# Optimization experiments

Measured on AMD Instinct MI355X. Metric: run time of the kernel, lower is better.

## Reference

```python
import jax, jax.numpy as jnp
import numpy as np

N_NODES = 50000
N_EDGES = 800000
C = 256
R = 4

def setup_inputs() -> dict:
    key = jax.random.key(0)
    ks = jax.random.split(key, 8)
    node_features = jax.random.normal(ks[0], (N_NODES, C), dtype=jnp.float32)
    edge_index = jax.random.randint(ks[1], (2, N_EDGES), 0, N_NODES, dtype=jnp.int64)
    edge_type = jax.random.randint(ks[2], (N_EDGES,), 0, R, dtype=jnp.int64)
    # RGCNConv params (glorot-ish scale)
    s = 1.0 / np.sqrt(C)
    rel_weight = jax.random.normal(ks[3], (R, C, C), dtype=jnp.float32) * s
    root_weight = jax.random.normal(ks[4], (C, C), dtype=jnp.float32) * s
    rgcn_bias = jax.random.normal(ks[5], (C,), dtype=jnp.float32) * 0.01
    att_weight = jax.random.normal(ks[6], (1, 2 * C), dtype=jnp.float32) * (1.0 / np.sqrt(2 * C))
    att_bias = jax.random.normal(ks[7], (1,), dtype=jnp.float32) * 0.01
    return {
        'node_features': node_features,
        'edge_index': edge_index,
        'edge_type': edge_type,
        'rel_weight': rel_weight,
        'root_weight': root_weight,
        'rgcn_bias': rgcn_bias,
        'att_weight': att_weight,
        'att_bias': att_bias,
    }


def _rgcn(node_features, edge_index, edge_type, rel_weight, root_weight, rgcn_bias):
    # PyG RGCNConv: per-relation mean aggregation of x_src @ W_r, plus root transform + bias.
    N = node_features.shape[0]
    src, dst = edge_index[0], edge_index[1]
    out = node_features @ root_weight + rgcn_bias  # [N, O]
    num_rel = rel_weight.shape[0]
    for r in range(num_rel):  # small fixed relation count
        trans = node_features @ rel_weight[r]          # [N, O] node-level transform
        mask = (edge_type == r)
        msg = jnp.where(mask[:, None], trans[src], 0.0)  # [E, O] masked gather
        ssum = jax.ops.segment_sum(msg, dst, num_segments=N)
        cnt = jax.ops.segment_sum(mask.astype(node_features.dtype), dst, num_segments=N)
        out = out + ssum / jnp.maximum(cnt, 1.0)[:, None]  # mean aggr; 0 where no edges
    return out


def reference(node_features, edge_index, edge_type, rel_weight, root_weight, rgcn_bias, att_weight, att_bias):
    u0 = _rgcn(node_features, edge_index, edge_type, rel_weight, root_weight, rgcn_bias)
    cat = jnp.concatenate([u0, node_features], axis=1)  # [N, 2O]
    a = jax.nn.sigmoid(cat @ att_weight.T + att_bias)   # [N, 1]
    h = jnp.tanh(u0) * a + node_features * (1.0 - a)
    return h
```

## Files before the change

kernel.cpp:

```cpp
#include <hip/hip_runtime.h>
#include <hip/hip_bf16.h>

#define C 256
#define NOUT 1280
#define BK 32

typedef __attribute__((ext_vector_type(8))) short bf16x8;
typedef __attribute__((ext_vector_type(4))) float f32x4;
typedef __attribute__((ext_vector_type(4))) unsigned short us4;

#define GLL16(g, l)                                                         \
  __builtin_amdgcn_global_load_lds(                                         \
      (const __attribute__((address_space(1))) void*)(g),                   \
      (__attribute__((address_space(3))) void*)(l), 16, 0, 0)

__device__ __forceinline__ float bf2f(unsigned short u) {
  return __uint_as_float(((unsigned int)u) << 16);
}
__device__ __forceinline__ unsigned short f2bf(float f) {
  unsigned int x = __float_as_uint(f);
  unsigned int lsb = (x >> 16) & 1u;
  x += 0x7fffu + lsb;
  return (unsigned short)(x >> 16);
}

__global__ void k_pre(const float* __restrict__ X, const float* __restrict__ rel,
                      const float* __restrict__ root, const float* __restrict__ attw,
                      unsigned short* __restrict__ Xbf, unsigned short* __restrict__ WT2,
                      float* __restrict__ ax2, int* __restrict__ cnt,
                      int N, int rowsPad) {
  __shared__ float tw[64][65];
  int b = blockIdx.x, t = threadIdx.x;
  if (b < 80) {
    int m = b >> 4, tile = b & 15;
    int ti = tile >> 2, tj = tile & 3;
    const float* W = (m == 0) ? root : (rel + (size_t)(m - 1) * C * C);
    int row = t >> 2, cj = (t & 3) * 16;
    const float* src = W + (size_t)(ti * 64 + row) * C + tj * 64 + cj;
#pragma unroll
    for (int j = 0; j < 4; ++j) {
      float4 v = reinterpret_cast<const float4*>(src)[j];
      tw[row][cj + j * 4 + 0] = v.x;
      tw[row][cj + j * 4 + 1] = v.y;
      tw[row][cj + j * 4 + 2] = v.z;
      tw[row][cj + j * 4 + 3] = v.w;
    }
    __syncthreads();
    int c = t >> 2, k0 = (t & 3) * 16;
    int n = m * 256 + tj * 64 + c;
    unsigned short o[16];
#pragma unroll
    for (int k = 0; k < 16; ++k) o[k] = f2bf(tw[k0 + k][c]);
#pragma unroll
    for (int j = 0; j < 4; ++j)
      *reinterpret_cast<us4*>(WT2 + (size_t)n * C + ti * 64 + k0 + j * 4) =
          *reinterpret_cast<us4*>(&o[j * 4]);
  } else if (b < 80 + (rowsPad >> 2)) {
    int row = (b - 80) * 4 + (t >> 6);
    int lane = t & 63;
    if (row < N) {
      float4 v = reinterpret_cast<const float4*>(X + (size_t)row * C)[lane];
      float4 w2 = reinterpret_cast<const float4*>(attw + C)[lane];
      us4 o;
      o.x = f2bf(v.x); o.y = f2bf(v.y); o.z = f2bf(v.z); o.w = f2bf(v.w);
      reinterpret_cast<us4*>(Xbf)[(size_t)row * 64 + lane] = o;
      float p = v.x * w2.x + v.y * w2.y + v.z * w2.z + v.w * w2.w;
#pragma unroll
      for (int m2 = 32; m2 >= 1; m2 >>= 1) p += __shfl_xor(p, m2);
      if (lane == 0) ax2[row] = p;
    } else if (row < rowsPad) {
      us4 z; z.x = 0; z.y = 0; z.z = 0; z.w = 0;
      reinterpret_cast<us4*>(Xbf)[(size_t)row * 64 + lane] = z;
      if (lane == 0) ax2[row] = 0.f;
    }
  } else {
    int i = (b - 80 - (rowsPad >> 2)) * 256 + t;
    if (i < N) cnt[i] = 0;
  }
}

__global__ void k_hist(const int* __restrict__ edst, int* __restrict__ cnt, int E) {
  int e = blockIdx.x * blockDim.x + threadIdx.x;
  if (e < E) atomicAdd(cnt + edst[e], 1);
}

__global__ void k_scan1(const int* __restrict__ cnt, int* __restrict__ rp,
                        int* __restrict__ bsum, int n) {
  __shared__ int s[512];
  int t = threadIdx.x;
  int i = blockIdx.x * 512 + t;
  int v = (i < n) ? cnt[i] : 0;
  s[t] = v;
  __syncthreads();
  for (int off = 1; off < 512; off <<= 1) {
    int add = (t >= off) ? s[t - off] : 0;
    __syncthreads();
    s[t] += add;
    __syncthreads();
  }
  if (i < n) rp[i] = s[t] - v;
  if (t == 511) bsum[blockIdx.x] = s[511];
}

__global__ void k_scan2(const int* __restrict__ bsum, int* __restrict__ boff,
                        int* __restrict__ rp, int nb, int n) {
  if (threadIdx.x == 0) {
    int run = 0;
    for (int b = 0; b < nb; ++b) { boff[b] = run; run += bsum[b]; }
    rp[n] = run;
  }
}

__global__ void k_scan3(int* __restrict__ rp, const int* __restrict__ boff,
                        int* __restrict__ cursor, int n) {
  int i = blockIdx.x * 512 + threadIdx.x;
  if (i < n) {
    int v = rp[i] + boff[blockIdx.x];
    rp[i] = v;
    cursor[i] = v;
  }
}

__global__ void k_fill(const int* __restrict__ esrc, const int* __restrict__ edst,
                       const int* __restrict__ etype, int* __restrict__ cursor,
                       unsigned int* __restrict__ sorted, int E) {
  int e = blockIdx.x * blockDim.x + threadIdx.x;
  if (e >= E) return;
  int d = edst[e];
  int pos = atomicAdd(cursor + d, 1);
  sorted[pos] = (unsigned int)esrc[e] | ((unsigned int)etype[e] << 28);
}

__global__ __launch_bounds__(256) void k_gemm(
    const unsigned short* __restrict__ Xbf, const unsigned short* __restrict__ WT2,
    unsigned short* __restrict__ Y, int rowsPad) {
  __shared__ unsigned short smem[16384];
  unsigned short* ldsA = smem;
  unsigned short* ldsB = smem + 8192;
  int tid = threadIdx.x;
  int wave = tid >> 6, lane = tid & 63;

  int nwg = gridDim.x, orig = blockIdx.x;
  int q = nwg >> 3, r = nwg & 7;
  int xcd = orig & 7, lin = orig >> 3;
  int wgid = (xcd < r ? xcd * (q + 1) : r * (q + 1) + (xcd - r) * q) + lin;
  int mblk = wgid / 10, nblk = wgid - mblk * 10;
  int row0 = mblk * 128, col0 = nblk * 128;
  int wr = wave >> 1, wc = wave & 1, lcol = lane & 15;

  const unsigned short* aSrc[2];
  const unsigned short* bSrc[2];
  int ldsOfs[2];
#pragma unroll
  for (int c2 = 0; c2 < 2; ++c2) {
    int off = (wave * 2 + c2) * 1024 + lane * 16;
    int rr = off >> 6;
    int lg8 = (((off >> 4) & 3) ^ ((rr >> 1) & 3)) * 8;
    aSrc[c2] = Xbf + (size_t)(row0 + rr) * C + lg8;
    bSrc[c2] = WT2 + (size_t)(col0 + rr) * C + lg8;
    ldsOfs[c2] = (wave * 2 + c2) * 1024;
  }

  int aoff[4], boff[4];
  int kb = (lane >> 4) * 16;
#pragma unroll
  for (int i = 0; i < 4; ++i) {
    int ar = wr * 64 + i * 16 + lcol;
    aoff[i] = ar * 64 + (kb ^ (((ar >> 1) & 3) << 4));
    int bc = wc * 64 + i * 16 + lcol;
    boff[i] = bc * 64 + (kb ^ (((bc >> 1) & 3) << 4));
  }

  f32x4 acc[4][4];
#pragma unroll
  for (int i = 0; i < 4; ++i)
#pragma unroll
    for (int j = 0; j < 4; ++j) {
      f32x4 z; z[0] = 0.f; z[1] = 0.f; z[2] = 0.f; z[3] = 0.f;
      acc[i][j] = z;
    }

  auto stage = [&](int buf, int ks) {
    int kofs = ks * BK;
#pragma unroll
    for (int c2 = 0; c2 < 2; ++c2) {
      GLL16(aSrc[c2] + kofs, (char*)(ldsA + buf * 4096) + ldsOfs[c2]);
      GLL16(bSrc[c2] + kofs, (char*)(ldsB + buf * 4096) + ldsOfs[c2]);
    }
  };

  stage(0, 0);
  __syncthreads();

#pragma unroll
  for (int ks = 0; ks < 8; ++ks) {
    int cur = ks & 1;
    if (ks + 1 < 8) stage(cur ^ 1, ks + 1);
    bf16x8 af[4], bfr[4];
#pragma unroll
    for (int i = 0; i < 4; ++i) {
      af[i]  = *reinterpret_cast<const bf16x8*>((const char*)(ldsA + cur * 4096) + aoff[i]);
      bfr[i] = *reinterpret_cast<const bf16x8*>((const char*)(ldsB + cur * 4096) + boff[i]);
    }
#pragma unroll
    for (int mr = 0; mr < 4; ++mr)
#pragma unroll
      for (int nc = 0; nc < 4; ++nc)
        acc[mr][nc] = __builtin_amdgcn_mfma_f32_16x16x32_bf16(af[mr], bfr[nc], acc[mr][nc], 0, 0, 0);
    __syncthreads();
  }

  int lrow4 = (lane >> 4) * 4;
#pragma unroll
  for (int mr = 0; mr < 4; ++mr)
#pragma unroll
    for (int nc = 0; nc < 4; ++nc)
#pragma unroll
      for (int reg = 0; reg < 4; ++reg) {
        int rr = wr * 64 + mr * 16 + lrow4 + reg;
        int cc = wc * 64 + nc * 16 + lcol;
        smem[rr * 128 + ((((cc >> 3) + rr) & 15) << 3) + (cc & 7)] =
            f2bf(acc[mr][nc][reg]);
      }
  __syncthreads();
#pragma unroll
  for (int rnd = 0; rnd < 8; ++rnd) {
    int rr = rnd * 16 + (tid >> 4);
    int g = tid & 15;
    int p = (g + rr) & 15;
    bf16x8 v = *reinterpret_cast<const bf16x8*>(smem + rr * 128 + p * 8);
    *reinterpret_cast<bf16x8*>(Y + (size_t)(row0 + rr) * NOUT + col0 + g * 8) = v;
  }
}

#define ACC(u, v)                                                            \
  do {                                                                       \
    float f0 = bf2f((v).x), f1 = bf2f((v).y), f2 = bf2f((v).z), f3 = bf2f((v).w); \
    switch ((u) >> 28) {                                                     \
      case 0: a0.x += f0; a0.y += f1; a0.z += f2; a0.w += f3; ++c0; break;   \
      case 1: a1.x += f0; a1.y += f1; a1.z += f2; a1.w += f3; ++c1; break;   \
      case 2: a2.x += f0; a2.y += f1; a2.z += f2; a2.w += f3; ++c2; break;   \
      default: a3.x += f0; a3.y += f1; a3.z += f2; a3.w += f3; ++c3; break;  \
    }                                                                        \
  } while (0)

__global__ void k_gg(const unsigned short* __restrict__ Y,
                     const unsigned int* __restrict__ sorted,
                     const int* __restrict__ rp, const float* __restrict__ X,
                     const float* __restrict__ bias, const float* __restrict__ attw,
                     const float* __restrict__ abp, const float* __restrict__ ax2,
                     float* __restrict__ out, int N) {
  int wave = threadIdx.x >> 6, lane = threadIdx.x & 63;
  int dst = blockIdx.x * 4 + wave;
  if (dst >= N) return;
  const us4* Yv = reinterpret_cast<const us4*>(Y);

  float4 a0 = make_float4(0, 0, 0, 0), a1 = a0, a2 = a0, a3 = a0;
  int c0 = 0, c1 = 0, c2 = 0, c3 = 0;
  int s = rp[dst], e2 = rp[dst + 1];

#define YIDX(u) ((size_t)((u) & 0x0FFFFFFFu) * 320 + (((u) >> 28) + 1) * 64 + lane)
  int e = s;
  for (; e + 8 <= e2; e += 8) {
    unsigned int u0 = sorted[e],     u1 = sorted[e + 1], u2 = sorted[e + 2], u3 = sorted[e + 3];
    unsigned int u4 = sorted[e + 4], u5 = sorted[e + 5], u6 = sorted[e + 6], u7 = sorted[e + 7];
    us4 v0 = Yv[YIDX(u0)], v1 = Yv[YIDX(u1)], v2 = Yv[YIDX(u2)], v3 = Yv[YIDX(u3)];
    us4 v4 = Yv[YIDX(u4)], v5 = Yv[YIDX(u5)], v6 = Yv[YIDX(u6)], v7 = Yv[YIDX(u7)];
    ACC(u0, v0); ACC(u1, v1); ACC(u2, v2); ACC(u3, v3);
    ACC(u4, v4); ACC(u5, v5); ACC(u6, v6); ACC(u7, v7);
  }
  for (; e + 4 <= e2; e += 4) {
    unsigned int u0 = sorted[e], u1 = sorted[e + 1], u2 = sorted[e + 2], u3 = sorted[e + 3];
    us4 v0 = Yv[YIDX(u0)], v1 = Yv[YIDX(u1)], v2 = Yv[YIDX(u2)], v3 = Yv[YIDX(u3)];
    ACC(u0, v0); ACC(u1, v1); ACC(u2, v2); ACC(u3, v3);
  }
  for (; e < e2; ++e) {
    unsigned int u = sorted[e];
    us4 v = Yv[YIDX(u)];
    ACC(u, v);
  }
#undef YIDX

  float s0 = 1.0f / (float)max(c0, 1);
  float s1 = 1.0f / (float)max(c1, 1);
  float s2 = 1.0f / (float)max(c2, 1);
  float s3 = 1.0f / (float)max(c3, 1);
  us4 rt = Yv[(size_t)dst * 320 + lane];
  float4 bi = reinterpret_cast<const float4*>(bias)[lane];
  float4 w1 = reinterpret_cast<const float4*>(attw)[lane];
  float4 u0;
  u0.x = a0.x * s0 + a1.x * s1 + a2.x * s2 + a3.x * s3 + bf2f(rt.x) + bi.x;
  u0.y = a0.y * s0 + a1.y * s1 + a2.y * s2 + a3.y * s3 + bf2f(rt.y) + bi.y;
  u0.z = a0.z * s0 + a1.z * s1 + a2.z * s2 + a3.z * s3 + bf2f(rt.z) + bi.z;
  u0.w = a0.w * s0 + a1.w * s1 + a2.w * s2 + a3.w * s3 + bf2f(rt.w) + bi.w;

  float p = u0.x * w1.x + u0.y * w1.y + u0.z * w1.z + u0.w * w1.w;
#pragma unroll
  for (int m2 = 32; m2 >= 1; m2 >>= 1) p += __shfl_xor(p, m2);
  float a = 1.0f / (1.0f + expf(-(p + ax2[dst] + abp[0])));
  float b = 1.0f - a;
  float4 x4 = reinterpret_cast<const float4*>(X + (size_t)dst * C)[lane];
  float4 h;
  h.x = tanhf(u0.x) * a + x4.x * b;
  h.y = tanhf(u0.y) * a + x4.y * b;
  h.z = tanhf(u0.z) * a + x4.z * b;
  h.w = tanhf(u0.w) * a + x4.w * b;
  reinterpret_cast<float4*>(out + (size_t)dst * C)[lane] = h;
}

extern "C" void kernel_launch(void* const* d_in, const int* in_sizes, int n_in,
                              void* d_out, int out_size, void* d_ws, size_t ws_size,
                              hipStream_t stream) {
  const float* X     = (const float*)d_in[0];
  const int*   eidx  = (const int*)d_in[1];
  const int*   etype = (const int*)d_in[2];
  const float* rel   = (const float*)d_in[3];
  const float* root  = (const float*)d_in[4];
  const float* bias  = (const float*)d_in[5];
  const float* attw  = (const float*)d_in[6];
  const float* ab    = (const float*)d_in[7];
  float* out = (float*)d_out;

  int N = in_sizes[0] / C;
  int E = in_sizes[2];
  int rowsPad = ((N + 127) / 128) * 128;
  const int* esrc = eidx;
  const int* edst = eidx + E;

  char* w = (char*)d_ws;
  size_t off = 0;
  auto alloc = [&](size_t bytes) -> void* {
    void* p = w + off;
    off += (bytes + 255) & ~(size_t)255;
    return p;
  };
  unsigned short* Y    = (unsigned short*)alloc((size_t)rowsPad * NOUT * 2);
  unsigned short* Xbf  = (unsigned short*)alloc((size_t)rowsPad * C * 2);
  unsigned short* WT2  = (unsigned short*)alloc((size_t)NOUT * C * 2);
  float* ax2  = (float*)alloc((size_t)rowsPad * 4);
  int* cnt    = (int*)alloc((size_t)N * 4);
  int* rp     = (int*)alloc((size_t)(N + 1) * 4);
  int* cursor = (int*)alloc((size_t)N * 4);
  int* bsum   = (int*)alloc(1024);
  int* boffb  = (int*)alloc(1024);
  unsigned int* sorted = (unsigned int*)alloc((size_t)E * 4);

  int preBlocks = 80 + (rowsPad >> 2) + (N + 255) / 256;
  k_pre<<<preBlocks, 256, 0, stream>>>(X, rel, root, attw, Xbf, WT2, ax2, cnt, N, rowsPad);
  k_hist<<<(E + 255) / 256, 256, 0, stream>>>(edst, cnt, E);
  int NB = (N + 511) / 512;
  k_scan1<<<NB, 512, 0, stream>>>(cnt, rp, bsum, N);
  k_scan2<<<1, 64, 0, stream>>>(bsum, boffb, rp, NB, N);
  k_scan3<<<NB, 512, 0, stream>>>(rp, boffb, cursor, N);
  k_fill<<<(E + 255) / 256, 256, 0, stream>>>(esrc, edst, etype, cursor, sorted, E);
  k_gemm<<<(rowsPad / 128) * 10, 256, 0, stream>>>(Xbf, WT2, Y, rowsPad);
  k_gg<<<(N + 3) / 4, 256, 0, stream>>>(Y, sorted, rp, X, bias, attw, ab, ax2, out, N);
}
```

Measured before the change: 254.8 us.

## Sort edges by (dst, relation) and precompute gather offsets to drop per-edge switch

The CSR is now bucketed by destination and relation (4N segments), so per-relation counts come from row pointers rather than per-edge counting. The gather kernel keeps one accumulator and applies a per-edge mean weight picked with compares, removing the four-way switch and the extra accumulator registers. The sorted array now stores a precomputed Y element offset instead of a packed src|type word. In exchange the histogram, scan and cursor arrays grow fourfold, and the scan must now cover 200k entries.

After: 251.8 us. About the same (-1.2%).

```diff
diff --git a/kernel.cpp b/kernel.cpp
--- a/kernel.cpp
+++ b/kernel.cpp
@@ -75,13 +75,14 @@
     }
   } else {
     int i = (b - 80 - (rowsPad >> 2)) * 256 + t;
-    if (i < N) cnt[i] = 0;
-  }
-}
-
-__global__ void k_hist(const int* __restrict__ edst, int* __restrict__ cnt, int E) {
+    if (i < 4 * N) cnt[i] = 0;
+  }
+}
+
+__global__ void k_hist(const int* __restrict__ edst, const int* __restrict__ etype,
+                       int* __restrict__ cnt, int E) {
   int e = blockIdx.x * blockDim.x + threadIdx.x;
-  if (e < E) atomicAdd(cnt + edst[e], 1);
+  if (e < E) atomicAdd(cnt + edst[e] * 4 + etype[e], 1);
 }
 
 __global__ void k_scan1(const int* __restrict__ cnt, int* __restrict__ rp,
@@ -127,8 +128,9 @@
   int e = blockIdx.x * blockDim.x + threadIdx.x;
   if (e >= E) return;
   int d = edst[e];
-  int pos = atomicAdd(cursor + d, 1);
-  sorted[pos] = (unsigned int)esrc[e] | ((unsigned int)etype[e] << 28);
+  int r = etype[e];
+  int pos = atomicAdd(cursor + d * 4 + r, 1);
+  sorted[pos] = (unsigned int)(esrc[e] * 320 + (r + 1) * 64);
 }
 
 __global__ __launch_bounds__(256) void k_gemm(
@@ -233,16 +235,10 @@
   }
 }
 
-#define ACC(u, v)                                                            \
-  do {                                                                       \
-    float f0 = bf2f((v).x), f1 = bf2f((v).y), f2 = bf2f((v).z), f3 = bf2f((v).w); \
-    switch ((u) >> 28) {                                                     \
-      case 0: a0.x += f0; a0.y += f1; a0.z += f2; a0.w += f3; ++c0; break;   \
-      case 1: a1.x += f0; a1.y += f1; a1.z += f2; a1.w += f3; ++c1; break;   \
-      case 2: a2.x += f0; a2.y += f1; a2.z += f2; a2.w += f3; ++c2; break;   \
-      default: a3.x += f0; a3.y += f1; a3.z += f2; a3.w += f3; ++c3; break;  \
-    }                                                                        \
-  } while (0)
+__device__ __forceinline__ float wsel(int e, int b1, int b2, int b3,
+                                      float s0, float s1, float s2, float s3) {
+  return e < b1 ? s0 : (e < b2 ? s1 : (e < b3 ? s2 : s3));
+}
 
 __global__ void k_gg(const unsigned short* __restrict__ Y,
                      const unsigned int* __restrict__ sorted,
@@ -255,56 +251,70 @@
   if (dst >= N) return;
   const us4* Yv = reinterpret_cast<const us4*>(Y);
 
-  float4 a0 = make_float4(0, 0, 0, 0), a1 = a0, a2 = a0, a3 = a0;
-  int c0 = 0, c1 = 0, c2 = 0, c3 = 0;
-  int s = rp[dst], e2 = rp[dst + 1];
-
-#define YIDX(u) ((size_t)((u) & 0x0FFFFFFFu) * 320 + (((u) >> 28) + 1) * 64 + lane)
-  int e = s;
-  for (; e + 8 <= e2; e += 8) {
+  int b0 = rp[dst * 4 + 0], b1 = rp[dst * 4 + 1], b2 = rp[dst * 4 + 2],
+      b3 = rp[dst * 4 + 3], b4 = rp[dst * 4 + 4];
+  float s0 = 1.0f / (float)max(b1 - b0, 1);
+  float s1 = 1.0f / (float)max(b2 - b1, 1);
+  float s2 = 1.0f / (float)max(b3 - b2, 1);
+  float s3 = 1.0f / (float)max(b4 - b3, 1);
+
+  float4 acc = make_float4(0.f, 0.f, 0.f, 0.f);
+
+  auto gstep = [&](unsigned int u, float wt) {
+    us4 v = Yv[(size_t)u + lane];
+    acc.x += wt * bf2f(v.x);
+    acc.y += wt * bf2f(v.y);
+    acc.z += wt * bf2f(v.z);
+    acc.w += wt * bf2f(v.w);
+  };
+
+  int e = b0;
+  for (; e + 8 <= b4; e += 8) {
     unsigned int u0 = sorted[e],     u1 = sorted[e + 1], u2 = sorted[e + 2], u3 = sorted[e + 3];
     unsigned int u4 = sorted[e + 4], u5 = sorted[e + 5], u6 = sorted[e + 6], u7 = sorted[e + 7];
-    us4 v0 = Yv[YIDX(u0)], v1 = Yv[YIDX(u1)], v2 = Yv[YIDX(u2)], v3 = Yv[YIDX(u3)];
-    us4 v4 = Yv[YIDX(u4)], v5 = Yv[YIDX(u5)], v6 = Yv[YIDX(u6)], v7 = Yv[YIDX(u7)];
-    ACC(u0, v0); ACC(u1, v1); ACC(u2, v2); ACC(u3, v3);
-    ACC(u4, v4); ACC(u5, v5); ACC(u6, v6); ACC(u7, v7);
-  }
-  for (; e + 4 <= e2; e += 4) {
+    float w0 = wsel(e + 0, b1, b2, b3, s0, s1, s2, s3);
+    float w1 = wsel(e + 1, b1, b2, b3, s0, s1, s2, s3);
+    float w2 = wsel(e + 2, b1, b2, b3, s0, s1, s2, s3);
+    float w3 = wsel(e + 3, b1, b2, b3, s0, s1, s2, s3);
+    float w4 = wsel(e + 4, b1, b2, b3, s0, s1, s2, s3);
+    float w5 = wsel(e + 5, b1, b2, b3, s0, s1, s2, s3);
+    float w6 = wsel(e + 6, b1, b2, b3, s0, s1, s2, s3);
+    float w7 = wsel(e + 7, b1, b2, b3, s0, s1, s2, s3);
+    gstep(u0, w0); gstep(u1, w1); gstep(u2, w2); gstep(u3, w3);
+    gstep(u4, w4); gstep(u5, w5); gstep(u6, w6); gstep(u7, w7);
+  }
+  for (; e + 4 <= b4; e += 4) {
     unsigned int u0 = sorted[e], u1 = sorted[e + 1], u2 = sorted[e + 2], u3 = sorted[e + 3];
-    us4 v0 = Yv[YIDX(u0)], v1 = Yv[YIDX(u1)], v2 = Yv[YIDX(u2)], v3 = Yv[YIDX(u3)];
-    ACC(u0, v0); ACC(u1, v1); ACC(u2, v2); ACC(u3, v3);
-  }
-  for (; e < e2; ++e) {
-    unsigned int u = sorted[e];
-    us4 v = Yv[YIDX(u)];
-    ACC(u, v);
-  }
-#undef YIDX
-
-  float s0 = 1.0f / (float)max(c0, 1);
-  float s1 = 1.0f / (float)max(c1, 1);
-  float s2 = 1.0f / (float)max(c2, 1);
-  float s3 = 1.0f / (float)max(c3, 1);
+    float w0 = wsel(e + 0, b1, b2, b3, s0, s1, s2, s3);
+    float w1 = wsel(e + 1, b1, b2, b3, s0, s1, s2, s3);
+    float w2 = wsel(e + 2, b1, b2, b3, s0, s1, s2, s3);
+    float w3 = wsel(e + 3, b1, b2, b3, s0, s1, s2, s3);
+    gstep(u0, w0); gstep(u1, w1); gstep(u2, w2); gstep(u3, w3);
+  }
+  for (; e < b4; ++e) {
+    gstep(sorted[e], wsel(e, b1, b2, b3, s0, s1, s2, s3));
+  }
+
   us4 rt = Yv[(size_t)dst * 320 + lane];
   float4 bi = reinterpret_cast<const float4*>(bias)[lane];
-  float4 w1 = reinterpret_cast<const float4*>(attw)[lane];
-  float4 u0;
-  u0.x = a0.x * s0 + a1.x * s1 + a2.x * s2 + a3.x * s3 + bf2f(rt.x) + bi.x;
-  u0.y = a0.y * s0 + a1.y * s1 + a2.y * s2 + a3.y * s3 + bf2f(rt.y) + bi.y;
-  u0.z = a0.z * s0 + a1.z * s1 + a2.z * s2 + a3.z * s3 + bf2f(rt.z) + bi.z;
-  u0.w = a0.w * s0 + a1.w * s1 + a2.w * s2 + a3.w * s3 + bf2f(rt.w) + bi.w;
-
-  float p = u0.x * w1.x + u0.y * w1.y + u0.z * w1.z + u0.w * w1.w;
+  float4 w1v = reinterpret_cast<const float4*>(attw)[lane];
+  float4 u0v;
+  u0v.x = acc.x + bf2f(rt.x) + bi.x;
+  u0v.y = acc.y + bf2f(rt.y) + bi.y;
+  u0v.z = acc.z + bf2f(rt.z) + bi.z;
+  u0v.w = acc.w + bf2f(rt.w) + bi.w;
+
+  float p = u0v.x * w1v.x + u0v.y * w1v.y + u0v.z * w1v.z + u0v.w * w1v.w;
 #pragma unroll
   for (int m2 = 32; m2 >= 1; m2 >>= 1) p += __shfl_xor(p, m2);
   float a = 1.0f / (1.0f + expf(-(p + ax2[dst] + abp[0])));
   float b = 1.0f - a;
   float4 x4 = reinterpret_cast<const float4*>(X + (size_t)dst * C)[lane];
   float4 h;
-  h.x = tanhf(u0.x) * a + x4.x * b;
-  h.y = tanhf(u0.y) * a + x4.y * b;
-  h.z = tanhf(u0.z) * a + x4.z * b;
-  h.w = tanhf(u0.w) * a + x4.w * b;
+  h.x = tanhf(u0v.x) * a + x4.x * b;
+  h.y = tanhf(u0v.y) * a + x4.y * b;
+  h.z = tanhf(u0v.z) * a + x4.z * b;
+  h.w = tanhf(u0v.w) * a + x4.w * b;
   reinterpret_cast<float4*>(out + (size_t)dst * C)[lane] = h;
 }
 
@@ -326,6 +336,7 @@
   int rowsPad = ((N + 127) / 128) * 128;
   const int* esrc = eidx;
   const int* edst = eidx + E;
+  int n4 = 4 * N;
 
   char* w = (char*)d_ws;
   size_t off = 0;
@@ -338,20 +349,20 @@
   unsigned short* Xbf  = (unsigned short*)alloc((size_t)rowsPad * C * 2);
   unsigned short* WT2  = (unsigned short*)alloc((size_t)NOUT * C * 2);
   float* ax2  = (float*)alloc((size_t)rowsPad * 4);
-  int* cnt    = (int*)alloc((size_t)N * 4);
-  int* rp     = (int*)alloc((size_t)(N + 1) * 4);
-  int* cursor = (int*)alloc((size_t)N * 4);
-  int* bsum   = (int*)alloc(1024);
-  int* boffb  = (int*)alloc(1024);
+  int* cnt    = (int*)alloc((size_t)n4 * 4);
+  int* rp     = (int*)alloc((size_t)(n4 + 1) * 4);
+  int* cursor = (int*)alloc((size_t)n4 * 4);
+  int* bsum   = (int*)alloc(2048);
+  int* boffb  = (int*)alloc(2048);
   unsigned int* sorted = (unsigned int*)alloc((size_t)E * 4);
 
-  int preBlocks = 80 + (rowsPad >> 2) + (N + 255) / 256;
+  int preBlocks = 80 + (rowsPad >> 2) + (n4 + 255) / 256;
   k_pre<<<preBlocks, 256, 0, stream>>>(X, rel, root, attw, Xbf, WT2, ax2, cnt, N, rowsPad);
-  k_hist<<<(E + 255) / 256, 256, 0, stream>>>(edst, cnt, E);
-  int NB = (N + 511) / 512;
-  k_scan1<<<NB, 512, 0, stream>>>(cnt, rp, bsum, N);
-  k_scan2<<<1, 64, 0, stream>>>(bsum, boffb, rp, NB, N);
-  k_scan3<<<NB, 512, 0, stream>>>(rp, boffb, cursor, N);
+  k_hist<<<(E + 255) / 256, 256, 0, stream>>>(edst, etype, cnt, E);
+  int NB = (n4 + 511) / 512;
+  k_scan1<<<NB, 512, 0, stream>>>(cnt, rp, bsum, n4);
+  k_scan2<<<1, 64, 0, stream>>>(bsum, boffb, rp, NB, n4);
+  k_scan3<<<NB, 512, 0, stream>>>(rp, boffb, cursor, n4);
   k_fill<<<(E + 255) / 256, 256, 0, stream>>>(esrc, edst, etype, cursor, sorted, E);
   k_gemm<<<(rowsPad / 128) * 10, 256, 0, stream>>>(Xbf, WT2, Y, rowsPad);
   k_gg<<<(N + 3) / 4, 256, 0, stream>>>(Y, sorted, rp, X, bias, attw, ab, ax2, out, N);
```
